# Kernel optimization log

Measured on AMD Instinct MI355X. Metric: run time of the kernel, lower is better.

Reference implementation:

```python
import jax, jax.numpy as jnp
import numpy as np

D_MODEL = 1024
D_FF = 4096
NUM_EXPERTS = 8
NUM_SLOTS = 2
LN_EPS = 1e-5


def setup_inputs() -> dict:
    key = jax.random.key(0)
    ks = jax.random.split(key, 4)
    x = jax.random.normal(ks[0], (4, 4096, D_MODEL), dtype=jnp.float32)
    slot_embeds = jax.random.normal(ks[1], (NUM_EXPERTS * NUM_SLOTS, D_MODEL), dtype=jnp.float32) * 0.02
    # per-expert MLP weights, stacked over expert axis (Linear bias=False)
    W1 = jax.random.normal(ks[2], (NUM_EXPERTS, D_MODEL, D_FF), dtype=jnp.float32) * (1.0 / np.sqrt(D_MODEL))
    W2 = jax.random.normal(ks[3], (NUM_EXPERTS, D_FF, D_MODEL), dtype=jnp.float32) * (1.0 / np.sqrt(D_FF))
    ln_gamma = jnp.ones((D_MODEL,), dtype=jnp.float32)
    ln_beta = jnp.zeros((D_MODEL,), dtype=jnp.float32)
    return {"x": x, "slot_embeds": slot_embeds, "W1": W1, "W2": W2,
            "ln_gamma": ln_gamma, "ln_beta": ln_beta}


def reference(x, slot_embeds, W1, W2, ln_gamma, ln_beta):
    B, T, D = x.shape
    E, S = NUM_EXPERTS, NUM_SLOTS
    # logits: [B, T, E*S]
    logits = jnp.einsum('btd,nd->btn', x, slot_embeds) / jnp.sqrt(jnp.asarray(D, x.dtype))
    # dispatch: softmax over tokens (dim=1)
    dispatch = jax.nn.softmax(logits, axis=1)
    slot_in = jnp.einsum('btn,btd->bnd', dispatch, x)  # [B, E*S, D]
    # LayerNorm over last dim
    mu = jnp.mean(slot_in, axis=-1, keepdims=True)
    var = jnp.mean(jnp.square(slot_in - mu), axis=-1, keepdims=True)
    h = (slot_in - mu) * jax.lax.rsqrt(var + LN_EPS) * ln_gamma + ln_beta
    # per-expert MLP as a single batched (grouped) GEMM pair
    h = h.reshape(B, E, S, D)
    u = jax.nn.gelu(jnp.einsum('besd,edf->besf', h, W1), approximate=False)
    slot_out = jnp.einsum('besf,efd->besd', u, W2).reshape(B, E * S, D)
    # combine: softmax over slots (dim=2)
    combine = jax.nn.softmax(logits, axis=2)
    return jnp.einsum('btn,bnd->btd', combine, slot_out)
```

## Files before the change

kernel.cpp:

```cpp
#include <hip/hip_runtime.h>
#include <math.h>

#define NB 4
#define NT 4096
#define ND 1024
#define NS 16
#define NE 8
#define NF 4096

__device__ __forceinline__ float gelu(float v) {
  return 0.5f * v * (1.f + erff(v * 0.70710678118654752f));
}

__global__ __launch_bounds__(256) void k_zero(float* __restrict__ p, int n) {
  int i = blockIdx.x * 256 + threadIdx.x;
  if (i < n) p[i] = 0.f;
}

__global__ __launch_bounds__(256) void k_logits(const float* __restrict__ x,
                                                const float* __restrict__ se,
                                                float* __restrict__ logits) {
  int wave = threadIdx.x >> 6, lane = threadIdx.x & 63;
  int g = blockIdx.x * 4 + wave;
  float acc[NS];
#pragma unroll
  for (int n = 0; n < NS; ++n) acc[n] = 0.f;
  const float* xr = x + (size_t)g * ND;
  for (int d = lane; d < ND; d += 64) {
    float xv = xr[d];
#pragma unroll
    for (int n = 0; n < NS; ++n) acc[n] += xv * se[n * ND + d];
  }
#pragma unroll
  for (int n = 0; n < NS; ++n) {
#pragma unroll
    for (int off = 32; off > 0; off >>= 1) acc[n] += __shfl_xor(acc[n], off, 64);
  }
  if (lane < NS) logits[(size_t)g * NS + lane] = acc[lane] * 0.03125f;
}

__global__ __launch_bounds__(256) void k_softmax_stats(const float* __restrict__ logits,
                                                       float* __restrict__ stats) {
  int bn = blockIdx.x;
  int b = bn >> 4, n = bn & 15;
  __shared__ float red[256];
  const float* lp = logits + ((size_t)b * NT) * NS + n;
  float m = -1e30f;
  for (int t = threadIdx.x; t < NT; t += 256) m = fmaxf(m, lp[(size_t)t * NS]);
  red[threadIdx.x] = m; __syncthreads();
  for (int s = 128; s > 0; s >>= 1) {
    if (threadIdx.x < s) red[threadIdx.x] = fmaxf(red[threadIdx.x], red[threadIdx.x + s]);
    __syncthreads();
  }
  m = red[0]; __syncthreads();
  float sm = 0.f;
  for (int t = threadIdx.x; t < NT; t += 256) sm += expf(lp[(size_t)t * NS] - m);
  red[threadIdx.x] = sm; __syncthreads();
  for (int s = 128; s > 0; s >>= 1) {
    if (threadIdx.x < s) red[threadIdx.x] += red[threadIdx.x + s];
    __syncthreads();
  }
  if (threadIdx.x == 0) { stats[bn * 2] = m; stats[bn * 2 + 1] = red[0]; }
}

__global__ __launch_bounds__(256) void k_slot_in(const float* __restrict__ x,
                                                 const float* __restrict__ logits,
                                                 const float* __restrict__ stats,
                                                 float* __restrict__ slot_in) {
  __shared__ float s_w[64 * NS];
  __shared__ float s_ms[NS * 2];
  int tc = blockIdx.x, dc = blockIdx.y, b = blockIdx.z;
  if (threadIdx.x < NS * 2) s_ms[threadIdx.x] = stats[b * NS * 2 + threadIdx.x];
  int d = dc * 256 + threadIdx.x;
  float acc[NS];
#pragma unroll
  for (int n = 0; n < NS; ++n) acc[n] = 0.f;
  __syncthreads();
  for (int t0 = tc * 256; t0 < tc * 256 + 256; t0 += 64) {
    __syncthreads();
    for (int i = threadIdx.x; i < 64 * NS; i += 256) {
      int n = i & 15;
      s_w[i] = expf(logits[((size_t)b * NT + t0) * NS + i] - s_ms[n * 2]) / s_ms[n * 2 + 1];
    }
    __syncthreads();
    for (int tt = 0; tt < 64; ++tt) {
      float xv = x[((size_t)b * NT + t0 + tt) * ND + d];
#pragma unroll
      for (int n = 0; n < NS; ++n) acc[n] += s_w[tt * NS + n] * xv;
    }
  }
#pragma unroll
  for (int n = 0; n < NS; ++n)
    atomicAdd(&slot_in[((size_t)b * NS + n) * ND + d], acc[n]);
}

__global__ __launch_bounds__(256) void k_layernorm(float* __restrict__ slot_in,
                                                   const float* __restrict__ gamma,
                                                   const float* __restrict__ beta) {
  int row = blockIdx.x;
  __shared__ float red[256];
  float* rp = slot_in + (size_t)row * ND;
  float v[4];
  float sum = 0.f;
#pragma unroll
  for (int j = 0; j < 4; ++j) { v[j] = rp[threadIdx.x + j * 256]; sum += v[j]; }
  red[threadIdx.x] = sum; __syncthreads();
  for (int s = 128; s > 0; s >>= 1) {
    if (threadIdx.x < s) red[threadIdx.x] += red[threadIdx.x + s];
    __syncthreads();
  }
  float mu = red[0] * (1.f / ND); __syncthreads();
  float vs = 0.f;
#pragma unroll
  for (int j = 0; j < 4; ++j) { float t = v[j] - mu; vs += t * t; }
  red[threadIdx.x] = vs; __syncthreads();
  for (int s = 128; s > 0; s >>= 1) {
    if (threadIdx.x < s) red[threadIdx.x] += red[threadIdx.x + s];
    __syncthreads();
  }
  float rstd = rsqrtf(red[0] * (1.f / ND) + 1e-5f);
#pragma unroll
  for (int j = 0; j < 4; ++j) {
    int dd = threadIdx.x + j * 256;
    rp[dd] = (v[j] - mu) * rstd * gamma[dd] + beta[dd];
  }
}

__global__ __launch_bounds__(256) void k_mlp1(const float* __restrict__ h,
                                              const float* __restrict__ W1,
                                              float* __restrict__ u) {
  __shared__ float s_h[8][512];
  int fc = blockIdx.x, dc = blockIdx.y, e = blockIdx.z;
  int f = fc * 256 + threadIdx.x;
  for (int i = threadIdx.x; i < 8 * 512; i += 256) {
    int bs = i >> 9, dd = i & 511;
    int b = bs >> 1, s = bs & 1;
    s_h[bs][dd] = h[((size_t)b * NS + (e * 2 + s)) * ND + dc * 512 + dd];
  }
  __syncthreads();
  float acc[8];
#pragma unroll
  for (int j = 0; j < 8; ++j) acc[j] = 0.f;
  const float* wp = W1 + ((size_t)e * ND + dc * 512) * NF + f;
  for (int dd = 0; dd < 512; ++dd) {
    float w = wp[(size_t)dd * NF];
#pragma unroll
    for (int j = 0; j < 8; ++j) acc[j] += s_h[j][dd] * w;
  }
#pragma unroll
  for (int j = 0; j < 8; ++j) {
    int b = j >> 1, s = j & 1;
    atomicAdd(&u[(((size_t)b * NE + e) * 2 + s) * NF + f], acc[j]);
  }
}

__global__ __launch_bounds__(256) void k_mlp2(const float* __restrict__ u,
                                              const float* __restrict__ W2,
                                              float* __restrict__ slot_out) {
  __shared__ float s_u[8][512];
  int fc = blockIdx.x, dc = blockIdx.y, e = blockIdx.z;
  int d = dc * 256 + threadIdx.x;
  for (int i = threadIdx.x; i < 8 * 512; i += 256) {
    int bs = i >> 9, ff = i & 511;
    int b = bs >> 1, s = bs & 1;
    s_u[bs][ff] = gelu(u[(((size_t)b * NE + e) * 2 + s) * NF + fc * 512 + ff]);
  }
  __syncthreads();
  float acc[8];
#pragma unroll
  for (int j = 0; j < 8; ++j) acc[j] = 0.f;
  const float* wp = W2 + ((size_t)e * NF + fc * 512) * ND + d;
  for (int ff = 0; ff < 512; ++ff) {
    float w = wp[(size_t)ff * ND];
#pragma unroll
    for (int j = 0; j < 8; ++j) acc[j] += s_u[j][ff] * w;
  }
#pragma unroll
  for (int j = 0; j < 8; ++j) {
    int b = j >> 1, s = j & 1;
    atomicAdd(&slot_out[((size_t)b * NS + (e * 2 + s)) * ND + d], acc[j]);
  }
}

__global__ __launch_bounds__(256) void k_combine(const float* __restrict__ logits,
                                                 const float* __restrict__ slot_out,
                                                 float* __restrict__ out) {
  int g = blockIdx.x;
  int b = g >> 12;
  __shared__ float s_l[NS];
  if (threadIdx.x < NS) s_l[threadIdx.x] = logits[(size_t)g * NS + threadIdx.x];
  __syncthreads();
  float m = -1e30f;
#pragma unroll
  for (int n = 0; n < NS; ++n) m = fmaxf(m, s_l[n]);
  float c[NS]; float sum = 0.f;
#pragma unroll
  for (int n = 0; n < NS; ++n) { c[n] = expf(s_l[n] - m); sum += c[n]; }
  float rs = 1.f / sum;
#pragma unroll
  for (int j = 0; j < 4; ++j) {
    int d = threadIdx.x + j * 256;
    float o = 0.f;
#pragma unroll
    for (int n = 0; n < NS; ++n) o += c[n] * slot_out[((size_t)b * NS + n) * ND + d];
    out[(size_t)g * ND + d] = o * rs;
  }
}

extern "C" void kernel_launch(void* const* d_in, const int* in_sizes, int n_in,
                              void* d_out, int out_size, void* d_ws, size_t ws_size,
                              hipStream_t stream) {
  const float* x     = (const float*)d_in[0];
  const float* se    = (const float*)d_in[1];
  const float* W1    = (const float*)d_in[2];
  const float* W2    = (const float*)d_in[3];
  const float* gamma = (const float*)d_in[4];
  const float* beta  = (const float*)d_in[5];
  float* out = (float*)d_out;

  float* ws       = (float*)d_ws;
  float* logits   = ws;
  float* stats    = ws + 262144;
  float* slot_in  = ws + 262400;
  float* slot_out = ws + 327936;
  float* u        = ws + 393472;

  k_zero<<<1536, 256, 0, stream>>>(slot_in, 393216);

  k_logits<<<NB * NT / 4, 256, 0, stream>>>(x, se, logits);
  k_softmax_stats<<<NB * NS, 256, 0, stream>>>(logits, stats);
  k_slot_in<<<dim3(16, 4, NB), 256, 0, stream>>>(x, logits, stats, slot_in);
  k_layernorm<<<NB * NS, 256, 0, stream>>>(slot_in, gamma, beta);
  k_mlp1<<<dim3(16, 2, NE), 256, 0, stream>>>(slot_in, W1, u);
  k_mlp2<<<dim3(8, 4, NE), 256, 0, stream>>>(u, W2, slot_out);
  k_combine<<<NB * NT, 256, 0, stream>>>(logits, slot_out, out);
}
```

Measured before the change: 513.8 us.

## Vectorize and retile logits, slot_in, MLP and combine kernels with shared-memory reuse

Rewrites most kernels. k_logits now caches slot embeddings in shared memory and computes 4 tokens per wave with float4 loads. k_combine caches slot_out in LDS, reuses each row's softmax across 4 tokens and writes float4 outputs. k_slot_in, k_mlp1 and k_mlp2 are retiled to use float4 weight and activation loads and spread work over many more blocks, which increases the number of atomicAdds and the split-K partial sums. The goal is to cut redundant global loads, raise parallelism and improve memory coalescing on the bandwidth-bound stages.

```diff
diff --git a/kernel.cpp b/kernel.cpp
--- a/kernel.cpp
+++ b/kernel.cpp
@@ -11,6 +11,9 @@
 __device__ __forceinline__ float gelu(float v) {
   return 0.5f * v * (1.f + erff(v * 0.70710678118654752f));
 }
+__device__ __forceinline__ void fma4(float4& a, float s, const float4& v) {
+  a.x += s * v.x; a.y += s * v.y; a.z += s * v.z; a.w += s * v.w;
+}
 
 __global__ __launch_bounds__(256) void k_zero(float* __restrict__ p, int n) {
   int i = blockIdx.x * 256 + threadIdx.x;
@@ -20,23 +23,43 @@
 __global__ __launch_bounds__(256) void k_logits(const float* __restrict__ x,
                                                 const float* __restrict__ se,
                                                 float* __restrict__ logits) {
-  int wave = threadIdx.x >> 6, lane = threadIdx.x & 63;
-  int g = blockIdx.x * 4 + wave;
-  float acc[NS];
-#pragma unroll
-  for (int n = 0; n < NS; ++n) acc[n] = 0.f;
-  const float* xr = x + (size_t)g * ND;
-  for (int d = lane; d < ND; d += 64) {
-    float xv = xr[d];
-#pragma unroll
-    for (int n = 0; n < NS; ++n) acc[n] += xv * se[n * ND + d];
-  }
-#pragma unroll
-  for (int n = 0; n < NS; ++n) {
-#pragma unroll
-    for (int off = 32; off > 0; off >>= 1) acc[n] += __shfl_xor(acc[n], off, 64);
-  }
-  if (lane < NS) logits[(size_t)g * NS + lane] = acc[lane] * 0.03125f;
+  __shared__ float s_se[NS * ND];
+  for (int i = threadIdx.x; i < NS * ND; i += 256) s_se[i] = se[i];
+  __syncthreads();
+  const int wave = threadIdx.x >> 6, lane = threadIdx.x & 63;
+  const int tbase = blockIdx.x * 64 + wave * 16;
+  for (int g = 0; g < 4; ++g) {
+    const int t0 = tbase + g * 4;
+    float acc[4][NS];
+#pragma unroll
+    for (int tt = 0; tt < 4; ++tt)
+#pragma unroll
+      for (int n = 0; n < NS; ++n) acc[tt][n] = 0.f;
+#pragma unroll
+    for (int it = 0; it < 4; ++it) {
+      const int d = it * 256 + lane * 4;
+      float4 xv[4];
+#pragma unroll
+      for (int tt = 0; tt < 4; ++tt)
+        xv[tt] = *reinterpret_cast<const float4*>(x + (size_t)(t0 + tt) * ND + d);
+#pragma unroll
+      for (int n = 0; n < NS; ++n) {
+        const float4 sv = *reinterpret_cast<const float4*>(&s_se[n * ND + d]);
+#pragma unroll
+        for (int tt = 0; tt < 4; ++tt)
+          acc[tt][n] += xv[tt].x * sv.x + xv[tt].y * sv.y + xv[tt].z * sv.z + xv[tt].w * sv.w;
+      }
+    }
+#pragma unroll
+    for (int tt = 0; tt < 4; ++tt)
+#pragma unroll
+      for (int n = 0; n < NS; ++n) {
+        float v = acc[tt][n];
+#pragma unroll
+        for (int off = 32; off > 0; off >>= 1) v += __shfl_xor(v, off, 64);
+        if (lane == n) logits[(size_t)(t0 + tt) * NS + n] = v * 0.03125f;
+      }
+  }
 }
 
 __global__ __launch_bounds__(256) void k_softmax_stats(const float* __restrict__ logits,
@@ -68,30 +91,29 @@
                                                  const float* __restrict__ stats,
                                                  float* __restrict__ slot_in) {
   __shared__ float s_w[64 * NS];
-  __shared__ float s_ms[NS * 2];
-  int tc = blockIdx.x, dc = blockIdx.y, b = blockIdx.z;
-  if (threadIdx.x < NS * 2) s_ms[threadIdx.x] = stats[b * NS * 2 + threadIdx.x];
-  int d = dc * 256 + threadIdx.x;
-  float acc[NS];
-#pragma unroll
-  for (int n = 0; n < NS; ++n) acc[n] = 0.f;
-  __syncthreads();
-  for (int t0 = tc * 256; t0 < tc * 256 + 256; t0 += 64) {
-    __syncthreads();
-    for (int i = threadIdx.x; i < 64 * NS; i += 256) {
-      int n = i & 15;
-      s_w[i] = expf(logits[((size_t)b * NT + t0) * NS + i] - s_ms[n * 2]) / s_ms[n * 2 + 1];
-    }
-    __syncthreads();
-    for (int tt = 0; tt < 64; ++tt) {
-      float xv = x[((size_t)b * NT + t0 + tt) * ND + d];
-#pragma unroll
-      for (int n = 0; n < NS; ++n) acc[n] += s_w[tt * NS + n] * xv;
-    }
-  }
-#pragma unroll
-  for (int n = 0; n < NS; ++n)
-    atomicAdd(&slot_in[((size_t)b * NS + n) * ND + d], acc[n]);
+  const int tc = blockIdx.x, b = blockIdx.y;
+  const int t0 = tc * 64;
+  for (int i = threadIdx.x; i < 64 * NS; i += 256) {
+    const int n = i & 15;
+    const float m = stats[(b * NS + n) * 2], s = stats[(b * NS + n) * 2 + 1];
+    s_w[i] = expf(logits[((size_t)b * NT + t0) * NS + i] - m) / s;
+  }
+  __syncthreads();
+  float4 acc[NS];
+#pragma unroll
+  for (int n = 0; n < NS; ++n) acc[n] = make_float4(0.f, 0.f, 0.f, 0.f);
+  const int d = threadIdx.x * 4;
+  for (int t = 0; t < 64; ++t) {
+    const float4 xv = *reinterpret_cast<const float4*>(x + ((size_t)b * NT + t0 + t) * ND + d);
+#pragma unroll
+    for (int n = 0; n < NS; ++n) fma4(acc[n], s_w[t * NS + n], xv);
+  }
+#pragma unroll
+  for (int n = 0; n < NS; ++n) {
+    float* dst = slot_in + ((size_t)b * NS + n) * ND + d;
+    atomicAdd(dst + 0, acc[n].x); atomicAdd(dst + 1, acc[n].y);
+    atomicAdd(dst + 2, acc[n].z); atomicAdd(dst + 3, acc[n].w);
+  }
 }
 
 __global__ __launch_bounds__(256) void k_layernorm(float* __restrict__ slot_in,
@@ -129,81 +151,114 @@
 __global__ __launch_bounds__(256) void k_mlp1(const float* __restrict__ h,
                                               const float* __restrict__ W1,
                                               float* __restrict__ u) {
-  __shared__ float s_h[8][512];
-  int fc = blockIdx.x, dc = blockIdx.y, e = blockIdx.z;
-  int f = fc * 256 + threadIdx.x;
-  for (int i = threadIdx.x; i < 8 * 512; i += 256) {
-    int bs = i >> 9, dd = i & 511;
-    int b = bs >> 1, s = bs & 1;
-    s_h[bs][dd] = h[((size_t)b * NS + (e * 2 + s)) * ND + dc * 512 + dd];
-  }
-  __syncthreads();
-  float acc[8];
-#pragma unroll
-  for (int j = 0; j < 8; ++j) acc[j] = 0.f;
-  const float* wp = W1 + ((size_t)e * ND + dc * 512) * NF + f;
-  for (int dd = 0; dd < 512; ++dd) {
-    float w = wp[(size_t)dd * NF];
-#pragma unroll
-    for (int j = 0; j < 8; ++j) acc[j] += s_h[j][dd] * w;
+  __shared__ float s_h[64][8];
+  const int ft = blockIdx.x, dc = blockIdx.y, e = blockIdx.z;
+  for (int i = threadIdx.x; i < 512; i += 256) {
+    const int dd = i >> 3, j = i & 7;
+    const int b = j >> 1, s = j & 1;
+    s_h[dd][j] = h[((size_t)b * NS + e * 2 + s) * ND + dc * 64 + dd];
+  }
+  __syncthreads();
+  float4 acc[8];
+#pragma unroll
+  for (int j = 0; j < 8; ++j) acc[j] = make_float4(0.f, 0.f, 0.f, 0.f);
+  const int f = ft * 1024 + threadIdx.x * 4;
+  const float* wbase = W1 + (size_t)(e * ND + dc * 64) * NF + f;
+  for (int dd = 0; dd < 64; ++dd) {
+    const float4 wv = *reinterpret_cast<const float4*>(wbase + (size_t)dd * NF);
+    const float4 h0 = *reinterpret_cast<const float4*>(&s_h[dd][0]);
+    const float4 h1 = *reinterpret_cast<const float4*>(&s_h[dd][4]);
+    fma4(acc[0], h0.x, wv); fma4(acc[1], h0.y, wv);
+    fma4(acc[2], h0.z, wv); fma4(acc[3], h0.w, wv);
+    fma4(acc[4], h1.x, wv); fma4(acc[5], h1.y, wv);
+    fma4(acc[6], h1.z, wv); fma4(acc[7], h1.w, wv);
   }
 #pragma unroll
   for (int j = 0; j < 8; ++j) {
-    int b = j >> 1, s = j & 1;
-    atomicAdd(&u[(((size_t)b * NE + e) * 2 + s) * NF + f], acc[j]);
+    const int b = j >> 1, s = j & 1;
+    float* dst = u + ((size_t)(b * NE + e) * 2 + s) * NF + f;
+    atomicAdd(dst + 0, acc[j].x); atomicAdd(dst + 1, acc[j].y);
+    atomicAdd(dst + 2, acc[j].z); atomicAdd(dst + 3, acc[j].w);
   }
 }
 
 __global__ __launch_bounds__(256) void k_mlp2(const float* __restrict__ u,
                                               const float* __restrict__ W2,
                                               float* __restrict__ slot_out) {
-  __shared__ float s_u[8][512];
-  int fc = blockIdx.x, dc = blockIdx.y, e = blockIdx.z;
-  int d = dc * 256 + threadIdx.x;
-  for (int i = threadIdx.x; i < 8 * 512; i += 256) {
-    int bs = i >> 9, ff = i & 511;
-    int b = bs >> 1, s = bs & 1;
-    s_u[bs][ff] = gelu(u[(((size_t)b * NE + e) * 2 + s) * NF + fc * 512 + ff]);
-  }
-  __syncthreads();
-  float acc[8];
-#pragma unroll
-  for (int j = 0; j < 8; ++j) acc[j] = 0.f;
-  const float* wp = W2 + ((size_t)e * NF + fc * 512) * ND + d;
-  for (int ff = 0; ff < 512; ++ff) {
-    float w = wp[(size_t)ff * ND];
-#pragma unroll
-    for (int j = 0; j < 8; ++j) acc[j] += s_u[j][ff] * w;
+  __shared__ float s_u[64][8];
+  const int fc = blockIdx.x, e = blockIdx.y;
+  for (int i = threadIdx.x; i < 512; i += 256) {
+    const int ff = i >> 3, j = i & 7;
+    const int b = j >> 1, s = j & 1;
+    s_u[ff][j] = gelu(u[((size_t)(b * NE + e) * 2 + s) * NF + fc * 64 + ff]);
+  }
+  __syncthreads();
+  float4 acc[8];
+#pragma unroll
+  for (int j = 0; j < 8; ++j) acc[j] = make_float4(0.f, 0.f, 0.f, 0.f);
+  const int d = threadIdx.x * 4;
+  const float* wbase = W2 + ((size_t)e * NF + fc * 64) * ND + d;
+  for (int ff = 0; ff < 64; ++ff) {
+    const float4 wv = *reinterpret_cast<const float4*>(wbase + (size_t)ff * ND);
+    const float4 u0 = *reinterpret_cast<const float4*>(&s_u[ff][0]);
+    const float4 u1 = *reinterpret_cast<const float4*>(&s_u[ff][4]);
+    fma4(acc[0], u0.x, wv); fma4(acc[1], u0.y, wv);
+    fma4(acc[2], u0.z, wv); fma4(acc[3], u0.w, wv);
+    fma4(acc[4], u1.x, wv); fma4(acc[5], u1.y, wv);
+    fma4(acc[6], u1.z, wv); fma4(acc[7], u1.w, wv);
   }
 #pragma unroll
   for (int j = 0; j < 8; ++j) {
-    int b = j >> 1, s = j & 1;
-    atomicAdd(&slot_out[((size_t)b * NS + (e * 2 + s)) * ND + d], acc[j]);
+    const int b = j >> 1, s = j & 1;
+    float* dst = slot_out + ((size_t)b * NS + e * 2 + s) * ND + d;
+    atomicAdd(dst + 0, acc[j].x); atomicAdd(dst + 1, acc[j].y);
+    atomicAdd(dst + 2, acc[j].z); atomicAdd(dst + 3, acc[j].w);
   }
 }
 
 __global__ __launch_bounds__(256) void k_combine(const float* __restrict__ logits,
                                                  const float* __restrict__ slot_out,
                                                  float* __restrict__ out) {
-  int g = blockIdx.x;
-  int b = g >> 12;
-  __shared__ float s_l[NS];
-  if (threadIdx.x < NS) s_l[threadIdx.x] = logits[(size_t)g * NS + threadIdx.x];
-  __syncthreads();
-  float m = -1e30f;
-#pragma unroll
-  for (int n = 0; n < NS; ++n) m = fmaxf(m, s_l[n]);
-  float c[NS]; float sum = 0.f;
-#pragma unroll
-  for (int n = 0; n < NS; ++n) { c[n] = expf(s_l[n] - m); sum += c[n]; }
-  float rs = 1.f / sum;
-#pragma unroll
-  for (int j = 0; j < 4; ++j) {
-    int d = threadIdx.x + j * 256;
-    float o = 0.f;
-#pragma unroll
-    for (int n = 0; n < NS; ++n) o += c[n] * slot_out[((size_t)b * NS + n) * ND + d];
-    out[(size_t)g * ND + d] = o * rs;
+  __shared__ float s_so[NS * ND];
+  const int tb = blockIdx.x, b = blockIdx.y;
+  for (int i = threadIdx.x; i < NS * ND; i += 256)
+    s_so[i] = slot_out[(size_t)b * NS * ND + i];
+  __syncthreads();
+  const int wave = threadIdx.x >> 6, lane = threadIdx.x & 63;
+  const int tbase = tb * 64 + wave * 16;
+  for (int g = 0; g < 4; ++g) {
+    const int t0 = tbase + g * 4;
+    float c[4][NS];
+#pragma unroll
+    for (int tt = 0; tt < 4; ++tt) {
+      const float* lp = logits + ((size_t)b * NT + t0 + tt) * NS;
+      float l[NS];
+      float m = -1e30f;
+#pragma unroll
+      for (int n = 0; n < NS; ++n) { l[n] = lp[n]; m = fmaxf(m, l[n]); }
+      float s = 0.f;
+#pragma unroll
+      for (int n = 0; n < NS; ++n) { l[n] = expf(l[n] - m); s += l[n]; }
+      const float rs = 1.f / s;
+#pragma unroll
+      for (int n = 0; n < NS; ++n) c[tt][n] = l[n] * rs;
+    }
+#pragma unroll
+    for (int it = 0; it < 4; ++it) {
+      const int d = it * 256 + lane * 4;
+      float4 acc[4];
+#pragma unroll
+      for (int tt = 0; tt < 4; ++tt) acc[tt] = make_float4(0.f, 0.f, 0.f, 0.f);
+#pragma unroll
+      for (int n = 0; n < NS; ++n) {
+        const float4 sv = *reinterpret_cast<const float4*>(&s_so[n * ND + d]);
+        fma4(acc[0], c[0][n], sv); fma4(acc[1], c[1][n], sv);
+        fma4(acc[2], c[2][n], sv); fma4(acc[3], c[3][n], sv);
+      }
+#pragma unroll
+      for (int tt = 0; tt < 4; ++tt)
+        *reinterpret_cast<float4*>(out + ((size_t)b * NT + t0 + tt) * ND + d) = acc[tt];
+    }
   }
 }
 
@@ -227,11 +282,11 @@
 
   k_zero<<<1536, 256, 0, stream>>>(slot_in, 393216);
 
-  k_logits<<<NB * NT / 4, 256, 0, stream>>>(x, se, logits);
+  k_logits<<<256, 256, 0, stream>>>(x, se, logits);
   k_softmax_stats<<<NB * NS, 256, 0, stream>>>(logits, stats);
-  k_slot_in<<<dim3(16, 4, NB), 256, 0, stream>>>(x, logits, stats, slot_in);
+  k_slot_in<<<dim3(64, NB), 256, 0, stream>>>(x, logits, stats, slot_in);
   k_layernorm<<<NB * NS, 256, 0, stream>>>(slot_in, gamma, beta);
-  k_mlp1<<<dim3(16, 2, NE), 256, 0, stream>>>(slot_in, W1, u);
-  k_mlp2<<<dim3(8, 4, NE), 256, 0, stream>>>(u, W2, slot_out);
-  k_combine<<<NB * NT, 256, 0, stream>>>(logits, slot_out, out);
-}
+  k_mlp1<<<dim3(4, 16, NE), 256, 0, stream>>>(slot_in, W1, u);
+  k_mlp2<<<dim3(64, NE), 256, 0, stream>>>(u, W2, slot_out);
+  k_combine<<<dim3(64, NB), 256, 0, stream>>>(logits, slot_out, out);
+}
```

Measured after the change: 626.8 us. 1.22x slower.
